# Performance work log

Hardware: AMD Instinct MI355X
Metric: run time of the kernel (lower is better)

Reference implementation:

```python
import jax, jax.numpy as jnp
import numpy as np


def setup_inputs() -> dict:
    key = jax.random.key(0)
    k1, k2, k3 = jax.random.split(key, 3)
    B, S, D = 4, 2048, 1024
    x = jax.random.normal(k1, (B, S, D), dtype=jnp.float32)
    # torch Linear weights: [out_features, in_features]
    w_qkv = jax.random.normal(k2, (3 * D, D), dtype=jnp.float32) * (D ** -0.5)
    w_out = jax.random.normal(k3, (D, D), dtype=jnp.float32) * (D ** -0.5)
    return {"x": x, "w_qkv": w_qkv, "w_out": w_out}


def reference(x, w_qkv, w_out):
    B, S, D = x.shape
    H = 16
    Dh = D // H
    qkv = jnp.einsum("bsd,ed->bse", x, w_qkv)  # [B,S,3D]
    q, k, v = jnp.split(qkv, 3, axis=-1)
    # [B,H,S,Dh]
    q = q.reshape(B, S, H, Dh).transpose(0, 2, 1, 3)
    k = k.reshape(B, S, H, Dh).transpose(0, 2, 1, 3)
    v = v.reshape(B, S, H, Dh).transpose(0, 2, 1, 3)
    scale = 1.0 / jnp.sqrt(jnp.asarray(Dh, dtype=x.dtype))
    scores = jnp.einsum("bhqd,bhkd->bhqk", q, k) * scale
    causal = jnp.tril(jnp.ones((S, S), dtype=bool))
    scores = jnp.where(causal, scores, jnp.finfo(scores.dtype).min)
    attn = jax.nn.softmax(scores, axis=-1)
    out = jnp.einsum("bhqk,bhkd->bhqd", attn, v)
    out = out.transpose(0, 2, 1, 3).reshape(B, S, D)
    return jnp.einsum("bsd,ed->bse", out, w_out)
```

## Files before the change

kernel.cpp:

```cpp
#include <hip/hip_runtime.h>
#include <stdint.h>

typedef __attribute__((ext_vector_type(8))) short short8;
typedef __attribute__((ext_vector_type(4))) float f32x4;
typedef __attribute__((ext_vector_type(16))) float f32x16;
typedef __attribute__((ext_vector_type(4))) unsigned int u32x4;

#define AS1 __attribute__((address_space(1)))
#define AS3 __attribute__((address_space(3)))

#define FSWZ(row) ((((row)) & 7) ^ (((row) >> 3) & 7))

#define KSCL 0.18033688f

__device__ __forceinline__ void gload_lds16(const void* g, void* l) {
  __builtin_amdgcn_global_load_lds((const AS1 void*)g, (AS3 void*)l, 16, 0, 0);
}

__device__ __forceinline__ short f2bf(float f) {
  uint32_t u = __float_as_uint(f);
  u += 0x7fffu + ((u >> 16) & 1u);
  return (short)(u >> 16);
}

__device__ __forceinline__ unsigned int cvtpk(float lo, float hi) {
  unsigned int r;
  asm("v_cvt_pk_bf16_f32 %0, %1, %2" : "=v"(r) : "v"(lo), "v"(hi));
  return r;
}

__global__ __launch_bounds__(256) void cvt_bf16(const float* __restrict__ in,
                                                short* __restrict__ out, int n8) {
  int i = blockIdx.x * 256 + threadIdx.x;
  if (i >= n8) return;
  const float4* p = (const float4*)(in + (size_t)i * 8);
  float4 a = p[0], b = p[1];
  short8 o;
  o[0] = f2bf(a.x); o[1] = f2bf(a.y); o[2] = f2bf(a.z); o[3] = f2bf(a.w);
  o[4] = f2bf(b.x); o[5] = f2bf(b.y); o[6] = f2bf(b.z); o[7] = f2bf(b.w);
  *(short8*)(out + (size_t)i * 8) = o;
}

__global__ __launch_bounds__(256) void gemm_bt(const short* __restrict__ A,
                                               const short* __restrict__ B,
                                               int K, int epi,
                                               short* __restrict__ q,
                                               short* __restrict__ k,
                                               short* __restrict__ v,
                                               float* __restrict__ outF, int N) {
  __shared__ short Al[128 * 64];
  __shared__ short Bl[128 * 64];
  const int tid = threadIdx.x;
  const int lane = tid & 63;
  const int wv = tid >> 6;
  const int wr = wv >> 1, wc = wv & 1;
  const int bm = blockIdx.y * 128, bn = blockIdx.x * 128;
  const int l15 = lane & 15, l4 = lane >> 4;

  f32x4 acc[4][4] = {};

  for (int kt = 0; kt < K; kt += 64) {
#pragma unroll
    for (int i = 0; i < 4; ++i) {
      int c = i * 256 + tid;
      int row = c >> 3, col = (c & 7) * 8;
      gload_lds16(A + (size_t)(bm + row) * K + kt + col, (char*)Al + (size_t)c * 16);
      gload_lds16(B + (size_t)(bn + row) * K + kt + col, (char*)Bl + (size_t)c * 16);
    }
    __syncthreads();
#pragma unroll
    for (int ks = 0; ks < 2; ++ks) {
      short8 af[4], bf[4];
#pragma unroll
      for (int mf = 0; mf < 4; ++mf)
        af[mf] = *(const short8*)&Al[(wr * 64 + mf * 16 + l15) * 64 + ks * 32 + l4 * 8];
#pragma unroll
      for (int nf = 0; nf < 4; ++nf)
        bf[nf] = *(const short8*)&Bl[(wc * 64 + nf * 16 + l15) * 64 + ks * 32 + l4 * 8];
#pragma unroll
      for (int mf = 0; mf < 4; ++mf)
#pragma unroll
        for (int nf = 0; nf < 4; ++nf)
          acc[mf][nf] =
              __builtin_amdgcn_mfma_f32_16x16x32_bf16(af[mf], bf[nf], acc[mf][nf], 0, 0, 0);
    }
    __syncthreads();
  }

  if (epi == 0) {
#pragma unroll
    for (int mf = 0; mf < 4; ++mf)
#pragma unroll
      for (int r = 0; r < 4; ++r) {
        int m = bm + wr * 64 + mf * 16 + l4 * 4 + r;
        int bb = m >> 11, s = m & 2047;
#pragma unroll
        for (int nf = 0; nf < 4; ++nf) {
          int n = bn + wc * 64 + nf * 16 + l15;
          int which = n >> 10, d = n & 1023, h = d >> 6, dh = d & 63;
          short* dst = (which == 0) ? q : ((which == 1) ? k : v);
          float val = acc[mf][nf][r];
          if (which == 1) val *= KSCL;
          dst[((size_t)(bb * 16 + h) * 2048 + s) * 64 + dh] = f2bf(val);
        }
      }
  } else {
#pragma unroll
    for (int mf = 0; mf < 4; ++mf)
#pragma unroll
      for (int r = 0; r < 4; ++r) {
        int m = bm + wr * 64 + mf * 16 + l4 * 4 + r;
#pragma unroll
        for (int nf = 0; nf < 4; ++nf) {
          int n = bn + wc * 64 + nf * 16 + l15;
          outF[(size_t)m * N + n] = acc[mf][nf][r];
        }
      }
  }
}

__global__ __launch_bounds__(256) void attn_fwd(const short* __restrict__ Qb,
                                                const short* __restrict__ Kb,
                                                const short* __restrict__ Vb,
                                                short* __restrict__ Ob) {
  __shared__ short Kl[2][64 * 64];
  __shared__ short Vt[2][64 * 64];
  const int tid = threadIdx.x, lane = tid & 63, wv = tid >> 6;
  const int l31 = lane & 31, l32 = lane >> 5;
  const int bh = blockIdx.x;
  const int qt = (int)gridDim.y - 1 - (int)blockIdx.y;
  const int b = bh >> 4, h = bh & 15;
  const size_t base = (size_t)bh * 2048 * 64;
  const int q0 = qt * 128;
  const int qw0 = q0 + wv * 32;
  const int qg = qw0 + l31;

  short8 qf[4];
#pragma unroll
  for (int dk = 0; dk < 4; ++dk)
    qf[dk] = *(const short8*)(Qb + base + (size_t)qg * 64 + dk * 16 + l32 * 8);

  f32x16 oacc[2] = {};
  float mrun = -1e30f, lrun = 0.f;
  short8 vv[2];

  const int nt = 2 * qt + 2;
#pragma unroll
  for (int i = 0; i < 2; ++i) {
    int c = i * 256 + tid;
    int row = c >> 3, j = c & 7;
    gload_lds16(Kb + base + (size_t)row * 64 + (j ^ FSWZ(row)) * 8,
                (char*)Kl[0] + (size_t)c * 16);
    vv[i] = *(const short8*)(Vb + base + (size_t)(c >> 3) * 64 + (c & 7) * 8);
  }

  for (int t = 0; t < nt; ++t) {
    const int cur = t & 1;
    const int kv0 = t * 64;
#pragma unroll
    for (int i = 0; i < 2; ++i) {
      int c = i * 256 + tid;
      int kr = c >> 3, c0 = (c & 7) * 8;
#pragma unroll
      for (int j = 0; j < 8; ++j) {
        int vr = c0 + j;
        Vt[cur][vr * 64 + (((kr >> 3) ^ FSWZ(vr)) * 8) + (kr & 7)] = vv[i][j];
      }
    }
    __syncthreads();

    if (t + 1 < nt) {
      const int kv1 = kv0 + 64;
#pragma unroll
      for (int i = 0; i < 2; ++i) {
        int c = i * 256 + tid;
        int row = c >> 3, j = c & 7;
        gload_lds16(Kb + base + (size_t)(kv1 + row) * 64 + (j ^ FSWZ(row)) * 8,
                    (char*)Kl[cur ^ 1] + (size_t)c * 16);
        vv[i] = *(const short8*)(Vb + base + (size_t)(kv1 + (c >> 3)) * 64 + (c & 7) * 8);
      }
    }

    if (kv0 <= qw0 + 31) {
      f32x16 sc[2] = {};
      __builtin_amdgcn_s_setprio(1);
#pragma unroll
      for (int dk = 0; dk < 4; ++dk)
#pragma unroll
        for (int kb = 0; kb < 2; ++kb) {
          int row = kb * 32 + l31;
          short8 kf =
              *(const short8*)&Kl[cur][row * 64 + (((dk * 2 + l32) ^ FSWZ(row)) * 8)];
          sc[kb] = __builtin_amdgcn_mfma_f32_32x32x16_bf16(kf, qf[dk], sc[kb], 0, 0, 0);
        }
      __builtin_amdgcn_s_setprio(0);

      const bool diag = (kv0 + 63 > qw0);
      float pp[2][16];
#pragma unroll
      for (int kb = 0; kb < 2; ++kb)
#pragma unroll
        for (int r = 0; r < 16; ++r) {
          float s = sc[kb][r];
          if (diag) {
            int kgl = kv0 + kb * 32 + (r & 3) + 8 * (r >> 2) + 4 * l32;
            if (kgl > qg) s = -1e30f;
          }
          pp[kb][r] = s;
        }
      float mx = -1e30f;
#pragma unroll
      for (int kb = 0; kb < 2; ++kb)
#pragma unroll
        for (int r = 0; r < 16; ++r) mx = fmaxf(mx, pp[kb][r]);
      mx = fmaxf(mx, __shfl_xor(mx, 32));
      if (!__all(mx - mrun <= 11.5416f)) {
        float mnew = fmaxf(mrun, mx);
        float alpha = exp2f(mrun - mnew);
        lrun *= alpha;
#pragma unroll
        for (int dt = 0; dt < 2; ++dt)
#pragma unroll
          for (int r = 0; r < 16; ++r) oacc[dt][r] *= alpha;
        mrun = mnew;
      }
      float ls = 0.f;
#pragma unroll
      for (int kb = 0; kb < 2; ++kb)
#pragma unroll
        for (int r = 0; r < 16; ++r) {
          float e = exp2f(pp[kb][r] - mrun);
          pp[kb][r] = e;
          ls += e;
        }
      ls += __shfl_xor(ls, 32);
      lrun += ls;

      unsigned int W[2][4][2];
#pragma unroll
      for (int kb = 0; kb < 2; ++kb)
#pragma unroll
        for (int g = 0; g < 4; ++g)
#pragma unroll
          for (int u = 0; u < 2; ++u)
            W[kb][g][u] = cvtpk(pp[kb][g * 4 + 2 * u], pp[kb][g * 4 + 2 * u + 1]);

      u32x4 pf[4];
#pragma unroll
      for (int kblk = 0; kblk < 4; ++kblk) {
        const int kbh = kblk >> 1;
#pragma unroll
        for (int u = 0; u < 2; ++u) {
          unsigned int A = W[kbh][2 * (kblk & 1)][u];
          unsigned int B = W[kbh][2 * (kblk & 1) + 1][u];
          unsigned int own = l32 ? B : A;
          unsigned int snd = l32 ? A : B;
          unsigned int rcv = (unsigned int)__shfl_xor((int)snd, 32);
          pf[kblk][0 + u] = l32 ? rcv : own;
          pf[kblk][2 + u] = l32 ? own : rcv;
        }
      }

      __builtin_amdgcn_s_setprio(1);
#pragma unroll
      for (int dt = 0; dt < 2; ++dt)
#pragma unroll
        for (int kblk = 0; kblk < 4; ++kblk) {
          int row = dt * 32 + l31;
          short8 vf =
              *(const short8*)&Vt[cur][row * 64 + (((kblk * 2 + l32) ^ FSWZ(row)) * 8)];
          oacc[dt] = __builtin_amdgcn_mfma_f32_32x32x16_bf16(
              vf, __builtin_bit_cast(short8, pf[kblk]), oacc[dt], 0, 0, 0);
        }
      __builtin_amdgcn_s_setprio(0);
    }
  }

  float inv = 1.f / lrun;
#pragma unroll
  for (int dt = 0; dt < 2; ++dt)
#pragma unroll
    for (int r = 0; r < 16; ++r) {
      int d = dt * 32 + (r & 3) + 8 * (r >> 2) + 4 * l32;
      Ob[(size_t)(b * 2048 + qg) * 1024 + h * 64 + d] = f2bf(oacc[dt][r] * inv);
    }
}

extern "C" void kernel_launch(void* const* d_in, const int* in_sizes, int n_in,
                              void* d_out, int out_size, void* d_ws, size_t ws_size,
                              hipStream_t stream) {
  const float* x = (const float*)d_in[0];
  const float* w_qkv = (const float*)d_in[1];
  const float* w_out = (const float*)d_in[2];
  float* out = (float*)d_out;

  char* ws = (char*)d_ws;
  const size_t MB = 1024 * 1024;
  short* xb    = (short*)(ws + 0 * MB);
  short* wqkvb = (short*)(ws + 16 * MB);
  short* woutb = (short*)(ws + 22 * MB);
  short* qb    = (short*)(ws + 24 * MB);
  short* kb    = (short*)(ws + 40 * MB);
  short* vb    = (short*)(ws + 56 * MB);
  short* ao    = xb;

  cvt_bf16<<<4096, 256, 0, stream>>>(x, xb, 8192 * 1024 / 8);
  cvt_bf16<<<1536, 256, 0, stream>>>(w_qkv, wqkvb, 3072 * 1024 / 8);
  cvt_bf16<<<512, 256, 0, stream>>>(w_out, woutb, 1024 * 1024 / 8);

  gemm_bt<<<dim3(3072 / 128, 8192 / 128), 256, 0, stream>>>(
      xb, wqkvb, 1024, 0, qb, kb, vb, nullptr, 3072);

  attn_fwd<<<dim3(64, 16), 256, 0, stream>>>(qb, kb, vb, ao);

  gemm_bt<<<dim3(1024 / 128, 8192 / 128), 256, 0, stream>>>(
      ao, woutb, 1024, 1, nullptr, nullptr, nullptr, out, 1024);
}
```

Measured before the change: 224.4 us.

## Load K fragments directly from global memory and tree-reduce softmax max/sum

Removes the K shared-memory double buffer and its async global-to-LDS loads, and has each wave read its K MFMA operands straight from global memory instead. This cuts LDS footprint and adds a min-blocks-per-CU launch bound of 4 to raise occupancy. It also replaces the serial max and sum reductions over the score registers with balanced trees to shorten the dependency chains. The risk is that the per-wave K loads are now uncoalesced and uncached in LDS, so they are repeated across the four waves and stall MFMA issue on memory latency.

```diff
diff --git a/kernel.cpp b/kernel.cpp
--- a/kernel.cpp
+++ b/kernel.cpp
@@ -119,11 +119,10 @@
   }
 }
 
-__global__ __launch_bounds__(256) void attn_fwd(const short* __restrict__ Qb,
-                                                const short* __restrict__ Kb,
-                                                const short* __restrict__ Vb,
-                                                short* __restrict__ Ob) {
-  __shared__ short Kl[2][64 * 64];
+__global__ __launch_bounds__(256, 4) void attn_fwd(const short* __restrict__ Qb,
+                                                   const short* __restrict__ Kb,
+                                                   const short* __restrict__ Vb,
+                                                   short* __restrict__ Ob) {
   __shared__ short Vt[2][64 * 64];
   const int tid = threadIdx.x, lane = tid & 63, wv = tid >> 6;
   const int l31 = lane & 31, l32 = lane >> 5;
@@ -148,9 +147,6 @@
 #pragma unroll
   for (int i = 0; i < 2; ++i) {
     int c = i * 256 + tid;
-    int row = c >> 3, j = c & 7;
-    gload_lds16(Kb + base + (size_t)row * 64 + (j ^ FSWZ(row)) * 8,
-                (char*)Kl[0] + (size_t)c * 16);
     vv[i] = *(const short8*)(Vb + base + (size_t)(c >> 3) * 64 + (c & 7) * 8);
   }
 
@@ -174,9 +170,6 @@
 #pragma unroll
       for (int i = 0; i < 2; ++i) {
         int c = i * 256 + tid;
-        int row = c >> 3, j = c & 7;
-        gload_lds16(Kb + base + (size_t)(kv1 + row) * 64 + (j ^ FSWZ(row)) * 8,
-                    (char*)Kl[cur ^ 1] + (size_t)c * 16);
         vv[i] = *(const short8*)(Vb + base + (size_t)(kv1 + (c >> 3)) * 64 + (c & 7) * 8);
       }
     }
@@ -188,9 +181,8 @@
       for (int dk = 0; dk < 4; ++dk)
 #pragma unroll
         for (int kb = 0; kb < 2; ++kb) {
-          int row = kb * 32 + l31;
-          short8 kf =
-              *(const short8*)&Kl[cur][row * 64 + (((dk * 2 + l32) ^ FSWZ(row)) * 8)];
+          short8 kf = *(const short8*)(Kb + base + (size_t)(kv0 + kb * 32 + l31) * 64 +
+                                       dk * 16 + l32 * 8);
           sc[kb] = __builtin_amdgcn_mfma_f32_32x32x16_bf16(kf, qf[dk], sc[kb], 0, 0, 0);
         }
       __builtin_amdgcn_s_setprio(0);
@@ -208,11 +200,13 @@
           }
           pp[kb][r] = s;
         }
-      float mx = -1e30f;
-#pragma unroll
-      for (int kb = 0; kb < 2; ++kb)
-#pragma unroll
-        for (int r = 0; r < 16; ++r) mx = fmaxf(mx, pp[kb][r]);
+      float m8[8];
+#pragma unroll
+      for (int i = 0; i < 8; ++i)
+        m8[i] = fmaxf(fmaxf(pp[0][i], pp[0][i + 8]), fmaxf(pp[1][i], pp[1][i + 8]));
+      float m4a = fmaxf(m8[0], m8[4]), m4b = fmaxf(m8[1], m8[5]);
+      float m4c = fmaxf(m8[2], m8[6]), m4d = fmaxf(m8[3], m8[7]);
+      float mx = fmaxf(fmaxf(m4a, m4b), fmaxf(m4c, m4d));
       mx = fmaxf(mx, __shfl_xor(mx, 32));
       if (!__all(mx - mrun <= 11.5416f)) {
         float mnew = fmaxf(mrun, mx);
@@ -224,15 +218,15 @@
           for (int r = 0; r < 16; ++r) oacc[dt][r] *= alpha;
         mrun = mnew;
       }
-      float ls = 0.f;
 #pragma unroll
       for (int kb = 0; kb < 2; ++kb)
 #pragma unroll
-        for (int r = 0; r < 16; ++r) {
-          float e = exp2f(pp[kb][r] - mrun);
-          pp[kb][r] = e;
-          ls += e;
-        }
+        for (int r = 0; r < 16; ++r) pp[kb][r] = exp2f(pp[kb][r] - mrun);
+      float s8[8];
+#pragma unroll
+      for (int i = 0; i < 8; ++i)
+        s8[i] = (pp[0][i] + pp[0][i + 8]) + (pp[1][i] + pp[1][i + 8]);
+      float ls = ((s8[0] + s8[4]) + (s8[1] + s8[5])) + ((s8[2] + s8[6]) + (s8[3] + s8[7]));
       ls += __shfl_xor(ls, 32);
       lrun += ls;
 
```

Measured after the change: 253.1 us. 12.8% more time.
